# Performance work log

Hardware: AMD Instinct MI355X
Metric: run time of the kernel (lower is better)

The kernel has to match this reference:

```python
import jax, jax.numpy as jnp
import numpy as np

N_NODES = 100000
N_EDGES = 1600000
FEAT_DIM = 128
EMBED_DIM = 32
N_CLASS_P1 = 17  # num_class + 1


def setup_inputs() -> dict:
    key = jax.random.key(0)
    ks = jax.random.split(key, 6)
    features = jax.random.normal(ks[0], (N_NODES, FEAT_DIM), dtype=jnp.float32)
    edges = jax.random.randint(ks[1], (N_EDGES, 2), 0, N_NODES, dtype=jnp.int64)
    weights = jax.random.uniform(ks[2], (N_EDGES,), dtype=jnp.float32)
    neighbours_sum = jax.random.uniform(ks[3], (N_NODES, 1), dtype=jnp.float32)
    W_embed = jax.random.normal(ks[4], (FEAT_DIM, EMBED_DIM), dtype=jnp.float32) / np.sqrt(FEAT_DIM)
    b_embed = jnp.zeros((EMBED_DIM,), dtype=jnp.float32)
    W_trans = jax.random.normal(ks[5], (2 * EMBED_DIM, N_CLASS_P1), dtype=jnp.float32) / np.sqrt(2 * EMBED_DIM)
    b_trans = jnp.zeros((N_CLASS_P1,), dtype=jnp.float32)
    return {
        "features": features, "edges": edges, "weights": weights,
        "neighbours_sum": neighbours_sum, "W_embed": W_embed, "b_embed": b_embed,
        "W_trans": W_trans, "b_trans": b_trans,
    }


def reference(features, edges, weights, neighbours_sum, W_embed, b_embed, W_trans, b_trans):
    num_nodes = features.shape[0]
    # node embedding: Linear(feature_dim -> num_dims)
    embed = features @ W_embed + b_embed               # [N, D]
    src_e = embed[edges[:, 0]]                         # [E, D] gather
    dst_e = embed[edges[:, 1]]                         # [E, D] gather
    # operator_sy1: [(src+dst)/2, (src-dst)^2]
    E_feat = jnp.concatenate([(src_e + dst_e) * 0.5, (src_e - dst_e) ** 2], axis=1)  # [E, 2D]
    poss_edge = jax.nn.softmax(E_feat @ W_trans + b_trans, axis=1)  # [E, C+1]
    # weighted scatter-add into nodes via edges[:,0]
    value = poss_edge * weights[:, None]
    recall_node = jax.ops.segment_sum(value, edges[:, 0], num_segments=num_nodes)  # [N, C+1]
    poss_node = recall_node / neighbours_sum
    return poss_node, poss_edge, recall_node
```

## Files before the change

### kernel.cpp

```cpp
#include <hip/hip_runtime.h>

#define NNODES 100000
#define NEDGES 1600000
#define FDIM 128
#define EDIM 32
#define NCLS 17
#define ROW 64

__global__ __launch_bounds__(256) void node_kernel(
    const float* __restrict__ features,
    const float* __restrict__ W_embed,
    const float* __restrict__ b_embed,
    const float* __restrict__ W_trans,
    float* __restrict__ nodetab)
{
  __shared__ float sW[FDIM * EDIM];
  __shared__ float sF[8 * FDIM];
  __shared__ float sE[8 * EDIM];
  __shared__ float sWt[2 * EDIM * NCLS];
  int tid = threadIdx.x;
  for (int i = tid; i < FDIM * EDIM / 4; i += 256)
    ((float4*)sW)[i] = ((const float4*)W_embed)[i];
  for (int i = tid; i < 2 * EDIM * NCLS; i += 256)
    sWt[i] = W_trans[i];
  int node0 = blockIdx.x * 8;
  ((float4*)sF)[tid] = ((const float4*)(features + (size_t)node0 * FDIM))[tid];
  __syncthreads();

  int n = tid >> 5, c = tid & 31;
  float acc = b_embed[c];
  const float* f = sF + n * FDIM;
  #pragma unroll 8
  for (int k = 0; k < FDIM; ++k)
    acc = fmaf(f[k], sW[k * EDIM + c], acc);
  int node = node0 + n;
  nodetab[(size_t)node * ROW + c] = acc;
  sE[n * EDIM + c] = acc;
  __syncthreads();

  if (c < NCLS) {
    const float* e = sE + n * EDIM;
    float lin = 0.f, sq = 0.f;
    #pragma unroll
    for (int k = 0; k < EDIM; ++k) {
      float ek = e[k];
      lin = fmaf(ek,      sWt[k * NCLS + c],          lin);
      sq  = fmaf(ek * ek, sWt[(EDIM + k) * NCLS + c], sq);
    }
    nodetab[(size_t)node * ROW + 32 + c] = 0.5f * lin + sq;
  }
}

__global__ __launch_bounds__(256, 4) void edge_kernel(
    const int*   __restrict__ edges,
    const float* __restrict__ weights,
    const float* __restrict__ W_trans,
    const float* __restrict__ b_trans,
    const float* __restrict__ nodetab,
    float* __restrict__ poss_edge,
    float* __restrict__ recall)
{
  __shared__ float sOut[256 * NCLS];
  __shared__ int   sSrc[256];
  int tid = threadIdx.x;
  int e = blockIdx.x * 256 + tid;
  int2 ed = ((const int2*)edges)[e];
  int src = ed.x, dst = ed.y;
  const float* rs = nodetab + (size_t)src * ROW;
  const float* rd = nodetab + (size_t)dst * ROW;

  float lgt[NCLS];
  #pragma unroll
  for (int c = 0; c < NCLS; ++c)
    lgt[c] = rs[32 + c] + rd[32 + c] + b_trans[c];

  #pragma unroll
  for (int k4 = 0; k4 < EDIM / 4; ++k4) {
    float4 a = ((const float4*)rs)[k4];
    float4 b = ((const float4*)rd)[k4];
    float p0 = -2.f * a.x * b.x, p1 = -2.f * a.y * b.y;
    float p2 = -2.f * a.z * b.z, p3 = -2.f * a.w * b.w;
    #pragma unroll
    for (int c = 0; c < NCLS; ++c) {
      lgt[c] = fmaf(p0, W_trans[(EDIM + 4 * k4 + 0) * NCLS + c], lgt[c]);
      lgt[c] = fmaf(p1, W_trans[(EDIM + 4 * k4 + 1) * NCLS + c], lgt[c]);
      lgt[c] = fmaf(p2, W_trans[(EDIM + 4 * k4 + 2) * NCLS + c], lgt[c]);
      lgt[c] = fmaf(p3, W_trans[(EDIM + 4 * k4 + 3) * NCLS + c], lgt[c]);
    }
  }

  float m = lgt[0];
  #pragma unroll
  for (int c = 1; c < NCLS; ++c) m = fmaxf(m, lgt[c]);
  float sum = 0.f;
  #pragma unroll
  for (int c = 0; c < NCLS; ++c) { lgt[c] = __expf(lgt[c] - m); sum += lgt[c]; }
  float inv = 1.0f / sum;
  float wi  = weights[e] * inv;

  sSrc[tid] = src;
  #pragma unroll
  for (int c = 0; c < NCLS; ++c) sOut[tid * NCLS + c] = lgt[c] * inv;
  __syncthreads();

  float4* outp = (float4*)(poss_edge + (size_t)blockIdx.x * 256 * NCLS);
  const float4* sOut4 = (const float4*)sOut;
  for (int i = tid; i < 256 * NCLS / 4; i += 256)
    outp[i] = sOut4[i];
  __syncthreads();

  #pragma unroll
  for (int c = 0; c < NCLS; ++c) sOut[tid * NCLS + c] = lgt[c] * wi;
  __syncthreads();

  for (int i = tid; i < 256 * NCLS; i += 256) {
    unsigned e2 = (unsigned)i / NCLS;
    unsigned c2 = (unsigned)i - e2 * NCLS;
    atomicAdd(recall + (size_t)sSrc[e2] * NCLS + c2, sOut[i]);
  }
}

__global__ __launch_bounds__(256) void div_kernel(
    const float* __restrict__ recall,
    const float* __restrict__ nsum,
    float* __restrict__ poss_node)
{
  int i = blockIdx.x * 256 + threadIdx.x;
  if (i < NNODES * NCLS)
    poss_node[i] = recall[i] / nsum[i / NCLS];
}

extern "C" void kernel_launch(void* const* d_in, const int* in_sizes, int n_in,
                              void* d_out, int out_size, void* d_ws, size_t ws_size,
                              hipStream_t stream) {
  const float* features = (const float*)d_in[0];
  const int*   edges    = (const int*)d_in[1];
  const float* weights  = (const float*)d_in[2];
  const float* nsum     = (const float*)d_in[3];
  const float* W_embed  = (const float*)d_in[4];
  const float* b_embed  = (const float*)d_in[5];
  const float* W_trans  = (const float*)d_in[6];
  const float* b_trans  = (const float*)d_in[7];

  float* out       = (float*)d_out;
  float* poss_node = out;
  float* poss_edge = out + (size_t)NNODES * NCLS;
  float* recall    = out + (size_t)(NNODES + NEDGES) * NCLS;
  float* nodetab   = (float*)d_ws;

  hipMemsetAsync(recall, 0, (size_t)NNODES * NCLS * sizeof(float), stream);
  node_kernel<<<NNODES / 8, 256, 0, stream>>>(features, W_embed, b_embed, W_trans, nodetab);
  edge_kernel<<<NEDGES / 256, 256, 0, stream>>>(edges, weights, W_trans, b_trans,
                                                nodetab, poss_edge, recall);
  div_kernel<<<(NNODES * NCLS + 255) / 256, 256, 0, stream>>>(recall, nsum, poss_node);
}
```

Measured before the change: 455.6 us.

## Store node table in bf16 and compute node embedding one node per thread

The per-node table, holding the embedding and the per-class linear/square terms, is packed as bf16 pairs. This halves the row from 256 to 128 bytes and so halves the random-gather traffic in the edge kernel. The node kernel is restructured so each thread computes a whole node's embedding in registers, reading the weights from global/constant cache instead of LDS. The risks are reduced precision in the logits and heavy register pressure in the node kernel, which has poorly coalesced per-thread feature reads.

```diff
diff --git a/kernel.cpp b/kernel.cpp
--- a/kernel.cpp
+++ b/kernel.cpp
@@ -5,50 +5,71 @@
 #define FDIM 128
 #define EDIM 32
 #define NCLS 17
-#define ROW 64
+#define ROWU 32
+
+typedef unsigned int u32;
+
+__device__ inline u32 bf16r(float x) {
+  u32 u = __float_as_uint(x);
+  return (u + 0x7FFFu + ((u >> 16) & 1u)) >> 16;
+}
+__device__ inline u32 pk(float lo, float hi) { return bf16r(lo) | (bf16r(hi) << 16); }
+__device__ inline float lo16(u32 u) { return __uint_as_float(u << 16); }
+__device__ inline float hi16(u32 u) { return __uint_as_float(u & 0xFFFF0000u); }
 
 __global__ __launch_bounds__(256) void node_kernel(
     const float* __restrict__ features,
     const float* __restrict__ W_embed,
     const float* __restrict__ b_embed,
     const float* __restrict__ W_trans,
-    float* __restrict__ nodetab)
+    u32* __restrict__ nodetab)
 {
-  __shared__ float sW[FDIM * EDIM];
-  __shared__ float sF[8 * FDIM];
-  __shared__ float sE[8 * EDIM];
-  __shared__ float sWt[2 * EDIM * NCLS];
-  int tid = threadIdx.x;
-  for (int i = tid; i < FDIM * EDIM / 4; i += 256)
-    ((float4*)sW)[i] = ((const float4*)W_embed)[i];
-  for (int i = tid; i < 2 * EDIM * NCLS; i += 256)
-    sWt[i] = W_trans[i];
-  int node0 = blockIdx.x * 8;
-  ((float4*)sF)[tid] = ((const float4*)(features + (size_t)node0 * FDIM))[tid];
-  __syncthreads();
+  int n = blockIdx.x * 256 + threadIdx.x;
+  if (n >= NNODES) return;
 
-  int n = tid >> 5, c = tid & 31;
-  float acc = b_embed[c];
-  const float* f = sF + n * FDIM;
-  #pragma unroll 8
-  for (int k = 0; k < FDIM; ++k)
-    acc = fmaf(f[k], sW[k * EDIM + c], acc);
-  int node = node0 + n;
-  nodetab[(size_t)node * ROW + c] = acc;
-  sE[n * EDIM + c] = acc;
-  __syncthreads();
+  float acc[EDIM];
+  #pragma unroll
+  for (int c = 0; c < EDIM; ++c) acc[c] = b_embed[c];
 
-  if (c < NCLS) {
-    const float* e = sE + n * EDIM;
-    float lin = 0.f, sq = 0.f;
+  const float4* f4 = (const float4*)(features + (size_t)n * FDIM);
+  for (int k4 = 0; k4 < FDIM / 4; ++k4) {
+    float4 f = f4[k4];
+    const float* w = W_embed + k4 * 4 * EDIM;
+    #pragma unroll
+    for (int c = 0; c < EDIM; ++c) {
+      acc[c] = fmaf(f.x, w[c],            acc[c]);
+      acc[c] = fmaf(f.y, w[EDIM + c],     acc[c]);
+      acc[c] = fmaf(f.z, w[2 * EDIM + c], acc[c]);
+      acc[c] = fmaf(f.w, w[3 * EDIM + c], acc[c]);
+    }
+  }
+
+  float sq[EDIM];
+  #pragma unroll
+  for (int k = 0; k < EDIM; ++k) sq[k] = acc[k] * acc[k];
+
+  float h[NCLS + 1];
+  #pragma unroll
+  for (int c = 0; c < NCLS; ++c) {
+    float lin = 0.f, sqs = 0.f;
     #pragma unroll
     for (int k = 0; k < EDIM; ++k) {
-      float ek = e[k];
-      lin = fmaf(ek,      sWt[k * NCLS + c],          lin);
-      sq  = fmaf(ek * ek, sWt[(EDIM + k) * NCLS + c], sq);
+      lin = fmaf(acc[k], W_trans[k * NCLS + c],          lin);
+      sqs = fmaf(sq[k],  W_trans[(EDIM + k) * NCLS + c], sqs);
     }
-    nodetab[(size_t)node * ROW + 32 + c] = 0.5f * lin + sq;
+    h[c] = 0.5f * lin + sqs;
   }
+  h[NCLS] = 0.f;
+
+  u32* row = nodetab + (size_t)n * ROWU;
+  u32 p[16];
+  #pragma unroll
+  for (int i = 0; i < 16; ++i) p[i] = pk(acc[2 * i], acc[2 * i + 1]);
+  #pragma unroll
+  for (int i = 0; i < 4; ++i)
+    ((uint4*)row)[i] = make_uint4(p[4 * i], p[4 * i + 1], p[4 * i + 2], p[4 * i + 3]);
+  #pragma unroll
+  for (int i = 0; i < 9; ++i) row[16 + i] = pk(h[2 * i], h[2 * i + 1]);
 }
 
 __global__ __launch_bounds__(256, 4) void edge_kernel(
@@ -56,7 +77,7 @@
     const float* __restrict__ weights,
     const float* __restrict__ W_trans,
     const float* __restrict__ b_trans,
-    const float* __restrict__ nodetab,
+    const u32*   __restrict__ nodetab,
     float* __restrict__ poss_edge,
     float* __restrict__ recall)
 {
@@ -66,26 +87,41 @@
   int e = blockIdx.x * 256 + tid;
   int2 ed = ((const int2*)edges)[e];
   int src = ed.x, dst = ed.y;
-  const float* rs = nodetab + (size_t)src * ROW;
-  const float* rd = nodetab + (size_t)dst * ROW;
+  const uint4* rs4 = (const uint4*)(nodetab + (size_t)src * ROWU);
+  const uint4* rd4 = (const uint4*)(nodetab + (size_t)dst * ROWU);
+
+  uint4 sh0 = rs4[4], dh0 = rd4[4];
+  uint4 sh1 = rs4[5], dh1 = rd4[5];
+  u32   sh2 = ((const u32*)rs4)[24], dh2 = ((const u32*)rd4)[24];
 
   float lgt[NCLS];
-  #pragma unroll
-  for (int c = 0; c < NCLS; ++c)
-    lgt[c] = rs[32 + c] + rd[32 + c] + b_trans[c];
+  {
+    u32 sp[9] = {sh0.x, sh0.y, sh0.z, sh0.w, sh1.x, sh1.y, sh1.z, sh1.w, sh2};
+    u32 dp[9] = {dh0.x, dh0.y, dh0.z, dh0.w, dh1.x, dh1.y, dh1.z, dh1.w, dh2};
+    #pragma unroll
+    for (int i = 0; i < 8; ++i) {
+      lgt[2 * i]     = lo16(sp[i]) + lo16(dp[i]) + b_trans[2 * i];
+      lgt[2 * i + 1] = hi16(sp[i]) + hi16(dp[i]) + b_trans[2 * i + 1];
+    }
+    lgt[16] = lo16(sp[8]) + lo16(dp[8]) + b_trans[16];
+  }
 
   #pragma unroll
-  for (int k4 = 0; k4 < EDIM / 4; ++k4) {
-    float4 a = ((const float4*)rs)[k4];
-    float4 b = ((const float4*)rd)[k4];
-    float p0 = -2.f * a.x * b.x, p1 = -2.f * a.y * b.y;
-    float p2 = -2.f * a.z * b.z, p3 = -2.f * a.w * b.w;
+  for (int q = 0; q < 4; ++q) {
+    uint4 sa = rs4[q], da = rd4[q];
+    u32 su[4] = {sa.x, sa.y, sa.z, sa.w};
+    u32 du[4] = {da.x, da.y, da.z, da.w};
+    float p[8];
     #pragma unroll
-    for (int c = 0; c < NCLS; ++c) {
-      lgt[c] = fmaf(p0, W_trans[(EDIM + 4 * k4 + 0) * NCLS + c], lgt[c]);
-      lgt[c] = fmaf(p1, W_trans[(EDIM + 4 * k4 + 1) * NCLS + c], lgt[c]);
-      lgt[c] = fmaf(p2, W_trans[(EDIM + 4 * k4 + 2) * NCLS + c], lgt[c]);
-      lgt[c] = fmaf(p3, W_trans[(EDIM + 4 * k4 + 3) * NCLS + c], lgt[c]);
+    for (int j = 0; j < 4; ++j) {
+      p[2 * j]     = -2.f * lo16(su[j]) * lo16(du[j]);
+      p[2 * j + 1] = -2.f * hi16(su[j]) * hi16(du[j]);
+    }
+    #pragma unroll
+    for (int j = 0; j < 8; ++j) {
+      const float* w = W_trans + (EDIM + q * 8 + j) * NCLS;
+      #pragma unroll
+      for (int c = 0; c < NCLS; ++c) lgt[c] = fmaf(p[j], w[c], lgt[c]);
     }
   }
 
@@ -146,10 +182,11 @@
   float* poss_node = out;
   float* poss_edge = out + (size_t)NNODES * NCLS;
   float* recall    = out + (size_t)(NNODES + NEDGES) * NCLS;
-  float* nodetab   = (float*)d_ws;
+  u32*   nodetab   = (u32*)d_ws;
 
   hipMemsetAsync(recall, 0, (size_t)NNODES * NCLS * sizeof(float), stream);
-  node_kernel<<<NNODES / 8, 256, 0, stream>>>(features, W_embed, b_embed, W_trans, nodetab);
+  node_kernel<<<(NNODES + 255) / 256, 256, 0, stream>>>(features, W_embed, b_embed,
+                                                        W_trans, nodetab);
   edge_kernel<<<NEDGES / 256, 256, 0, stream>>>(edges, weights, W_trans, b_trans,
                                                 nodetab, poss_edge, recall);
   div_kernel<<<(NNODES * NCLS + 255) / 256, 256, 0, stream>>>(recall, nsum, poss_node);
```

Measured after the change: 447.7 us. Within noise of the previous version (-1.7%).
